# Kernel tuning notes

Measured on AMD Instinct MI355X. Metric: run time of the kernel, lower is better.

Reference implementation:

```python
import jax, jax.numpy as jnp
import numpy as np

N, E, F_IN, NUM_GRAPHS, K = 50000, 500000, 160, 128, 3


def _glorot(k, shape):
    lim = np.sqrt(6.0 / (shape[-2] + shape[-1])).astype(np.float32)
    return jax.random.uniform(k, shape, jnp.float32, -lim, lim)


def setup_inputs() -> dict:
    key = jax.random.key(0)
    ks = jax.random.split(key, 8)
    x = jax.random.normal(ks[0], (N, F_IN), jnp.float32)
    edge_index = jax.random.randint(ks[1], (2, E), 0, N)
    edge_attr = jax.random.uniform(ks[2], (E,), jnp.float32)
    batch = jnp.sort(jax.random.randint(ks[3], (N,), 0, NUM_GRAPHS))
    W1 = _glorot(ks[4], (K, F_IN, 128)); b1 = jnp.zeros((128,), jnp.float32)
    W2 = _glorot(ks[5], (K, 128, 64)); b2 = jnp.zeros((64,), jnp.float32)
    W3 = _glorot(ks[6], (K, 64, 32)); b3 = jnp.zeros((32,), jnp.float32)
    Wl = _glorot(ks[7], (32, 2)); bl = jnp.zeros((2,), jnp.float32)
    return dict(x=x, edge_index=edge_index, edge_attr=edge_attr, batch=batch,
                W1=W1, b1=b1, W2=W2, b2=b2, W3=W3, b3=b3, Wl=Wl, bl=bl)


def _cheb_norm(src, dst, edge_attr, n):
    # PyG ChebConv: sym-normalized Laplacian, lambda_max=2 =>
    # L_hat = (2/lmax)*L_sym - I = -D^{-1/2} A D^{-1/2} (diagonal = 0)
    deg = jax.ops.segment_sum(edge_attr, src, num_segments=n)
    safe = jnp.where(deg > 0, deg, 1.0)
    dinv = jnp.where(deg > 0, jax.lax.rsqrt(safe), 0.0)
    return -dinv[src] * edge_attr * dinv[dst]


def _propagate(x, src, dst, w, n):
    # out[dst] += w * x[src]  (sparse L_hat @ x)
    return jax.ops.segment_sum(w[:, None] * x[src], dst, num_segments=n)


def _cheb_conv(x, src, dst, w, W, b, n):
    # Chebyshev recurrence: T0 = x, T1 = L_hat x, Tk = 2 L_hat T(k-1) - T(k-2)
    tx0 = x
    out = tx0 @ W[0]
    tx1 = _propagate(tx0, src, dst, w, n)
    out = out + tx1 @ W[1]
    for k in range(2, W.shape[0]):
        tx2 = 2.0 * _propagate(tx1, src, dst, w, n) - tx0
        out = out + tx2 @ W[k]
        tx0, tx1 = tx1, tx2
    return out + b


def reference(x, edge_index, edge_attr, batch, W1, b1, W2, b2, W3, b3, Wl, bl):
    n = x.shape[0]
    src, dst = edge_index[0], edge_index[1]
    w = _cheb_norm(src, dst, edge_attr, n)
    h = jax.nn.relu(_cheb_conv(x, src, dst, w, W1, b1, n))
    h = jax.nn.relu(_cheb_conv(h, src, dst, w, W2, b2, n))
    h = jax.nn.relu(_cheb_conv(h, src, dst, w, W3, b3, n))
    # global_mean_pool over graph ids (dropout omitted: eval mode)
    sums = jax.ops.segment_sum(h, batch, num_segments=NUM_GRAPHS)
    cnt = jax.ops.segment_sum(jnp.ones((n,), h.dtype), batch, num_segments=NUM_GRAPHS)
    pooled = sums / jnp.maximum(cnt, 1.0)[:, None]
    return pooled @ Wl + bl
```

## Files before the change

kernel.cpp:

```cpp
#include <hip/hip_runtime.h>

#define N_NODES 50000
#define N_EDGES 500000
#define NUM_G   128
#define SCAN_NB 49
#define PN      (SCAN_NB * 1024)
#define NCX     64
#define ECH     7813
#define RNG     8192
#define NRY     7
#define HVB     (2 * NCX * NRY)
#define CONVB   7813
#define WPREPB  360
#define SCVB    (NCX * NRY)
#define GEMM_MB 782

typedef __attribute__((ext_vector_type(8))) short short8;
typedef __attribute__((ext_vector_type(4))) float f32x4;

__device__ __forceinline__ unsigned f2bf(float x) {
    unsigned u = __float_as_uint(x);
    return (u + 0x7FFFu + ((u >> 16) & 1u)) >> 16;
}
__device__ __forceinline__ float bf2f(unsigned h) {
    return __uint_as_float(h << 16);
}

__device__ __forceinline__ void wprep_one(const float* __restrict__ W, unsigned short* __restrict__ WT,
                                          int t, int FIN, int F) {
    int n = t / FIN, k = t - n * FIN;
    int sel = n / F, c = n - sel * F;
    float v;
    if (sel == 0) v = W[(size_t)k * F + c] - W[(size_t)2 * FIN * F + (size_t)k * F + c];
    else          v = W[(size_t)sel * FIN * F + (size_t)k * F + c];
    WT[t] = (unsigned short)f2bf(v);
}

__global__ __launch_bounds__(256)
void prep_kernel(const int* __restrict__ src, const int* __restrict__ dst,
                 const float* __restrict__ ea,
                 float* __restrict__ pdeg, int* __restrict__ pcnt,
                 const float* __restrict__ x, unsigned short* __restrict__ Xb,
                 const float* __restrict__ W1, const float* __restrict__ W2,
                 const float* __restrict__ W3,
                 unsigned short* __restrict__ WT1, unsigned short* __restrict__ WT2,
                 unsigned short* __restrict__ WT3) {
    __shared__ unsigned lh[RNG];
    int vb = blockIdx.x, tid = threadIdx.x;
    if (vb < HVB) {
        bool isdeg = vb < NCX * NRY;
        int v2 = isdeg ? vb : vb - NCX * NRY;
        int xk = v2 & 63, y = v2 >> 6;
        int base = y * RNG;
        for (int i = tid; i < RNG; i += 256) lh[i] = 0u;
        __syncthreads();
        int e0 = xk * ECH, e1 = min(e0 + ECH, N_EDGES);
        if (isdeg) {
            for (int e = e0 + tid; e < e1; e += 256) {
                int s = src[e];
                if ((unsigned)(s - base) < RNG) atomicAdd((float*)&lh[s - base], ea[e]);
            }
        } else {
            for (int e = e0 + tid; e < e1; e += 256) {
                int d = dst[e];
                if ((unsigned)(d - base) < RNG) atomicAdd((int*)&lh[d - base], 1);
            }
        }
        __syncthreads();
        if (isdeg) {
            for (int i = tid; i < RNG; i += 256) {
                int n = base + i;
                if (n < PN) pdeg[(size_t)xk * PN + n] = ((float*)lh)[i];
            }
        } else {
            for (int i = tid; i < RNG; i += 256) {
                int n = base + i;
                if (n < PN) pcnt[(size_t)xk * PN + n] = ((int*)lh)[i];
            }
        }
    } else if (vb < HVB + CONVB) {
        int t = (vb - HVB) * 256 + tid;
        if (t < N_NODES * 160 / 4) {
            float4 v = reinterpret_cast<const float4*>(x)[t];
            ushort4 r;
            r.x = (unsigned short)f2bf(v.x);
            r.y = (unsigned short)f2bf(v.y);
            r.z = (unsigned short)f2bf(v.z);
            r.w = (unsigned short)f2bf(v.w);
            *reinterpret_cast<ushort4*>(Xb + (size_t)t * 4) = r;
        }
    } else {
        int t = (vb - HVB - CONVB) * 256 + tid;
        if (t < 61440)      wprep_one(W1, WT1, t, 160, 128);
        else if (t < 86016) wprep_one(W2, WT2, t - 61440, 128, 64);
        else if (t < 92160) wprep_one(W3, WT3, t - 86016, 64, 32);
    }
}

__global__ __launch_bounds__(256)
void reduce_scan_kernel(const float* __restrict__ pdeg, int* __restrict__ pcnt,
                        float* __restrict__ dinv, int* __restrict__ cnt,
                        int* __restrict__ partial) {
    int b = blockIdx.x, t = threadIdx.x;
    int i0 = b * 1024 + t * 4;
    float d0 = 0.f, d1 = 0.f, d2 = 0.f, d3 = 0.f;
    int r0 = 0, r1 = 0, r2 = 0, r3 = 0;
    for (int x = 0; x < NCX; ++x) {
        float4 pv = *reinterpret_cast<const float4*>(pdeg + (size_t)x * PN + i0);
        int4   cv = *reinterpret_cast<const int4*>(pcnt + (size_t)x * PN + i0);
        *reinterpret_cast<int4*>(pcnt + (size_t)x * PN + i0) = make_int4(r0, r1, r2, r3);
        d0 += pv.x; d1 += pv.y; d2 += pv.z; d3 += pv.w;
        r0 += cv.x; r1 += cv.y; r2 += cv.z; r3 += cv.w;
    }
    float dd[4] = {d0, d1, d2, d3};
    int   rr[4] = {r0, r1, r2, r3};
    int s = 0;
    #pragma unroll
    for (int j = 0; j < 4; ++j) {
        int n = i0 + j;
        if (n < N_NODES) {
            float dv = dd[j], r = 0.f;
            if (dv > 0.f) {
                r = rsqrtf(dv);
                r = r * (1.5f - 0.5f * dv * r * r);
            }
            dinv[n] = r;
            cnt[n] = rr[j];
            s += rr[j];
        } else {
            cnt[n] = 0;
        }
    }
    __shared__ int red[256];
    red[t] = s;
    __syncthreads();
    for (int off = 128; off > 0; off >>= 1) {
        if (t < off) red[t] += red[t + off];
        __syncthreads();
    }
    if (t == 0) partial[b] = red[0];
}

__global__ __launch_bounds__(256)
void scan_final_kernel(const int* __restrict__ cnt, const int* __restrict__ partial,
                       int* __restrict__ rowptr, int n) {
    int b = blockIdx.x, t = threadIdx.x;
    __shared__ int red[256];
    __shared__ int sh_off, sh_tot;
    if (t < 64) {
        int orig = (t < SCAN_NB) ? partial[t] : 0;
        int v = orig;
        #pragma unroll
        for (int off = 1; off < 64; off <<= 1) {
            int u = __shfl_up(v, off, 64);
            if (t >= off) v += u;
        }
        if (t == b) sh_off = v - orig;
        if (t == SCAN_NB - 1) sh_tot = v;
    }
    __syncthreads();
    int4 v = reinterpret_cast<const int4*>(cnt)[b * 256 + t];
    int s = v.x + v.y + v.z + v.w;
    red[t] = s;
    __syncthreads();
    for (int off = 1; off < 256; off <<= 1) {
        int u = (t >= off) ? red[t - off] : 0;
        __syncthreads();
        red[t] += u;
        __syncthreads();
    }
    int excl = sh_off + ((t == 0) ? 0 : red[t - 1]);
    int i0 = b * 1024 + t * 4;
    if (i0 < n)     rowptr[i0]     = excl;
    if (i0 + 1 < n) rowptr[i0 + 1] = excl + v.x;
    if (i0 + 2 < n) rowptr[i0 + 2] = excl + v.x + v.y;
    if (i0 + 3 < n) rowptr[i0 + 3] = excl + v.x + v.y + v.z;
    if (b == SCAN_NB - 1 && t == 0) rowptr[n] = sh_tot;
}

__device__ void scatter_body(int vb, const int* __restrict__ src, const int* __restrict__ dst,
                             const float* __restrict__ ea,
                             const int* __restrict__ rowptr, const int* __restrict__ pcnt,
                             int2* __restrict__ csr, unsigned char* smraw) {
    int* cursor = (int*)smraw;
    int tid = threadIdx.x;
    int x = vb & 63, y = vb >> 6;
    int base = y * RNG;
    for (int i = tid; i < RNG; i += 256) {
        int n = base + i;
        cursor[i] = (n < N_NODES) ? (rowptr[n] + pcnt[(size_t)x * PN + n]) : 0;
    }
    __syncthreads();
    int e0 = x * ECH, e1 = min(e0 + ECH, N_EDGES);
    for (int e = e0 + tid; e < e1; e += 256) {
        int d = dst[e];
        if ((unsigned)(d - base) < RNG) {
            int pos = atomicAdd(&cursor[d - base], 1);
            int2 ew;
            ew.x = src[e];
            ew.y = __float_as_int(ea[e]);
            csr[pos] = ew;
        }
    }
}

template<int FIN, int F>
__device__ void gemm_body(int bx, int g, const unsigned short* __restrict__ Xb,
                          const unsigned short* __restrict__ WT, const float* __restrict__ dinv,
                          unsigned short* __restrict__ Y0, unsigned short* __restrict__ Y1,
                          unsigned short* __restrict__ Y2, int nrows, unsigned char* smraw) {
    constexpr int KT = FIN / 32;
    constexpr int NT = F / 32;
    constexpr int SA = FIN + 8;
    constexpr int F8 = FIN / 8;
    short* Bs = (short*)smraw;

    int tid = threadIdx.x;
    int lane = tid & 63, w = tid >> 6;
    int m0 = bx * 64;
    unsigned short* Ys = (g == 0) ? Y0 : (g == 1) ? Y1 : Y2;

    int colb = lane & 15;
    int q8 = (lane >> 4) << 3;
    int rq = (lane >> 4) << 2;
    int arow = m0 + w * 16 + colb;
    bool rok = arow < nrows;

    short8 afr[KT];
    #pragma unroll
    for (int kt = 0; kt < KT; ++kt) {
        short8 z = {0, 0, 0, 0, 0, 0, 0, 0};
        afr[kt] = rok ? *reinterpret_cast<const short8*>(Xb + (size_t)arow * FIN + (kt << 5) + q8) : z;
    }

    for (int nt = 0; nt < NT; ++nt) {
        int n0 = (g * NT + nt) << 5;
        __syncthreads();
        for (int span = tid; span < 32 * F8; span += 256) {
            int r = span / F8, c8 = (span - r * F8) << 3;
            int pr = (r < 16) ? (r << 1) : (((r - 16) << 1) + 1);
            *reinterpret_cast<uint4*>(&Bs[r * SA + c8]) =
                *reinterpret_cast<const uint4*>(WT + (size_t)(n0 + pr) * FIN + c8);
        }
        __syncthreads();

        f32x4 acc0 = {0.f, 0.f, 0.f, 0.f}, acc1 = acc0;
        #pragma unroll
        for (int kt = 0; kt < KT; ++kt) {
            short8 b0 = *reinterpret_cast<const short8*>(&Bs[colb * SA + (kt << 5) + q8]);
            short8 b1 = *reinterpret_cast<const short8*>(&Bs[(colb + 16) * SA + (kt << 5) + q8]);
            acc0 = __builtin_amdgcn_mfma_f32_16x16x32_bf16(afr[kt], b0, acc0, 0, 0, 0);
            acc1 = __builtin_amdgcn_mfma_f32_16x16x32_bf16(afr[kt], b1, acc1, 0, 0, 0);
        }

        int lc = (nt << 5) + (colb << 1);
        #pragma unroll
        for (int r = 0; r < 4; ++r) {
            int orow = m0 + w * 16 + rq + r;
            if (orow < nrows) {
                float sc = (g == 2) ? dinv[orow] : 1.0f;
                unsigned pack = f2bf(acc0[r] * sc) | (f2bf(acc1[r] * sc) << 16);
                *reinterpret_cast<unsigned*>(Ys + (size_t)orow * F + lc) = pack;
            }
        }
    }
}

__global__ __launch_bounds__(256)
void sg_kernel(const int* __restrict__ src, const int* __restrict__ dst,
               const float* __restrict__ ea,
               const int* __restrict__ rowptr, const int* __restrict__ pcnt,
               int2* __restrict__ csr,
               const unsigned short* __restrict__ Xb, const unsigned short* __restrict__ WT1,
               const float* __restrict__ dinv,
               unsigned short* __restrict__ Y0, unsigned short* __restrict__ Y1,
               unsigned short* __restrict__ Y2) {
    __shared__ alignas(16) unsigned char sm[32768];
    int vb = blockIdx.x;
    if (vb < SCVB) {
        scatter_body(vb, src, dst, ea, rowptr, pcnt, csr, sm);
    } else {
        int v2 = vb - SCVB;
        gemm_body<160, 128>(v2 % GEMM_MB, v2 / GEMM_MB, Xb, WT1, dinv, Y0, Y1, Y2, N_NODES, sm);
    }
}

template<int FIN, int F>
__launch_bounds__(256)
__global__ void cheb_gemm(const unsigned short* __restrict__ Xb, const unsigned short* __restrict__ WT,
                          const float* __restrict__ dinv,
                          unsigned short* __restrict__ Y0, unsigned short* __restrict__ Y1,
                          unsigned short* __restrict__ Y2, int nrows) {
    __shared__ alignas(16) unsigned char sm[32 * (FIN + 8) * 2];
    gemm_body<FIN, F>(blockIdx.x, blockIdx.y, Xb, WT, dinv, Y0, Y1, Y2, nrows, sm);
}

__device__ __forceinline__ void acc8(float* acc, uint4 p, float wv) {
    acc[0] += wv * bf2f(p.x & 0xFFFFu);
    acc[1] += wv * __uint_as_float(p.x & 0xFFFF0000u);
    acc[2] += wv * bf2f(p.y & 0xFFFFu);
    acc[3] += wv * __uint_as_float(p.y & 0xFFFF0000u);
    acc[4] += wv * bf2f(p.z & 0xFFFFu);
    acc[5] += wv * __uint_as_float(p.z & 0xFFFF0000u);
    acc[6] += wv * bf2f(p.w & 0xFFFFu);
    acc[7] += wv * __uint_as_float(p.w & 0xFFFF0000u);
}

__device__ __forceinline__ void expand8(uint4 p, float* o) {
    o[0] = bf2f(p.x & 0xFFFFu);
    o[1] = __uint_as_float(p.x & 0xFFFF0000u);
    o[2] = bf2f(p.y & 0xFFFFu);
    o[3] = __uint_as_float(p.y & 0xFFFF0000u);
    o[4] = bf2f(p.z & 0xFFFFu);
    o[5] = __uint_as_float(p.z & 0xFFFF0000u);
    o[6] = bf2f(p.w & 0xFFFFu);
    o[7] = __uint_as_float(p.w & 0xFFFF0000u);
}

template<int F, int MODE>
__launch_bounds__(256)
__global__ void gather_kernel(const unsigned short* __restrict__ X, const int2* __restrict__ csr,
                              const int* __restrict__ rowptr, const float* __restrict__ dinv,
                              const unsigned short* __restrict__ Y, const float* __restrict__ bias,
                              unsigned short* __restrict__ O, int n) {
    constexpr int FQ8 = F >> 3;
    constexpr int DPB = 256 / FQ8;
    constexpr int CAP = 2048;
    __shared__ int2 scsr[CAP];
    __shared__ int srp[DPB + 1];
    int tid = threadIdx.x;
    int db0 = blockIdx.x * DPB;
    if (tid <= DPB) srp[tid] = rowptr[min(db0 + tid, n)];
    __syncthreads();
    int ebeg = srp[0];
    int ecnt = srp[DPB] - ebeg;
    bool staged = ecnt <= CAP;
    if (staged) {
        for (int i = tid; i < ecnt; i += 256)
            scsr[i] = csr[ebeg + i];
    }
    __syncthreads();

    int d = db0 + tid / FQ8;
    if (d >= n) return;
    int f8 = (tid % FQ8) << 3;
    float acc[8] = {0.f, 0.f, 0.f, 0.f, 0.f, 0.f, 0.f, 0.f};

    if (staged) {
        int beg = srp[tid / FQ8] - ebeg, end = srp[tid / FQ8 + 1] - ebeg;
        int i = beg;
        for (; i + 7 < end; i += 8) {
            int2 e0 = scsr[i],     e1 = scsr[i + 1], e2 = scsr[i + 2], e3 = scsr[i + 3];
            int2 e4 = scsr[i + 4], e5 = scsr[i + 5], e6 = scsr[i + 6], e7 = scsr[i + 7];
            uint4 p0 = *reinterpret_cast<const uint4*>(X + (size_t)e0.x * F + f8);
            uint4 p1 = *reinterpret_cast<const uint4*>(X + (size_t)e1.x * F + f8);
            uint4 p2 = *reinterpret_cast<const uint4*>(X + (size_t)e2.x * F + f8);
            uint4 p3 = *reinterpret_cast<const uint4*>(X + (size_t)e3.x * F + f8);
            uint4 p4 = *reinterpret_cast<const uint4*>(X + (size_t)e4.x * F + f8);
            uint4 p5 = *reinterpret_cast<const uint4*>(X + (size_t)e5.x * F + f8);
            uint4 p6 = *reinterpret_cast<const uint4*>(X + (size_t)e6.x * F + f8);
            uint4 p7 = *reinterpret_cast<const uint4*>(X + (size_t)e7.x * F + f8);
            acc8(acc, p0, __int_as_float(e0.y));
            acc8(acc, p1, __int_as_float(e1.y));
            acc8(acc, p2, __int_as_float(e2.y));
            acc8(acc, p3, __int_as_float(e3.y));
            acc8(acc, p4, __int_as_float(e4.y));
            acc8(acc, p5, __int_as_float(e5.y));
            acc8(acc, p6, __int_as_float(e6.y));
            acc8(acc, p7, __int_as_float(e7.y));
        }
        for (; i + 3 < end; i += 4) {
            int2 e0 = scsr[i], e1 = scsr[i + 1], e2 = scsr[i + 2], e3 = scsr[i + 3];
            uint4 p0 = *reinterpret_cast<const uint4*>(X + (size_t)e0.x * F + f8);
            uint4 p1 = *reinterpret_cast<const uint4*>(X + (size_t)e1.x * F + f8);
            uint4 p2 = *reinterpret_cast<const uint4*>(X + (size_t)e2.x * F + f8);
            uint4 p3 = *reinterpret_cast<const uint4*>(X + (size_t)e3.x * F + f8);
            acc8(acc, p0, __int_as_float(e0.y));
            acc8(acc, p1, __int_as_float(e1.y));
            acc8(acc, p2, __int_as_float(e2.y));
            acc8(acc, p3, __int_as_float(e3.y));
        }
        for (; i < end; ++i) {
            int2 e = scsr[i];
            uint4 p = *reinterpret_cast<const uint4*>(X + (size_t)e.x * F + f8);
            acc8(acc, p, __int_as_float(e.y));
        }
    } else {
        int beg = srp[tid / FQ8], end = srp[tid / FQ8 + 1];
        for (int i = beg; i < end; ++i) {
            int2 e = csr[i];
            uint4 p = *reinterpret_cast<const uint4*>(X + (size_t)e.x * F + f8);
            acc8(acc, p, __int_as_float(e.y));
        }
    }

    float y[8];
    expand8(*reinterpret_cast<const uint4*>(Y + (size_t)d * F + f8), y);
    float dv = dinv[d];
    float v[8];
    if (MODE == 0) {
        float dv2 = 2.f * dv;
        #pragma unroll
        for (int j = 0; j < 8; ++j) v[j] = dv * (y[j] - dv2 * acc[j]);
    } else {
        float4 ba = *reinterpret_cast<const float4*>(bias + f8);
        float4 bb = *reinterpret_cast<const float4*>(bias + f8 + 4);
        v[0] = fmaxf(y[0] - dv * acc[0] + ba.x, 0.f);
        v[1] = fmaxf(y[1] - dv * acc[1] + ba.y, 0.f);
        v[2] = fmaxf(y[2] - dv * acc[2] + ba.z, 0.f);
        v[3] = fmaxf(y[3] - dv * acc[3] + ba.w, 0.f);
        v[4] = fmaxf(y[4] - dv * acc[4] + bb.x, 0.f);
        v[5] = fmaxf(y[5] - dv * acc[5] + bb.y, 0.f);
        v[6] = fmaxf(y[6] - dv * acc[6] + bb.z, 0.f);
        v[7] = fmaxf(y[7] - dv * acc[7] + bb.w, 0.f);
    }
    uint4 o;
    o.x = f2bf(v[0]) | (f2bf(v[1]) << 16);
    o.y = f2bf(v[2]) | (f2bf(v[3]) << 16);
    o.z = f2bf(v[4]) | (f2bf(v[5]) << 16);
    o.w = f2bf(v[6]) | (f2bf(v[7]) << 16);
    *reinterpret_cast<uint4*>(O + (size_t)d * F + f8) = o;
}

__device__ __forceinline__ int lower_bound_dev(const int* __restrict__ a, int n, int v) {
    int lo = 0, hi = n;
    while (lo < hi) {
        int mid = (lo + hi) >> 1;
        if (a[mid] < v) lo = mid + 1; else hi = mid;
    }
    return lo;
}

__global__ void pool_kernel(const unsigned short* __restrict__ H, const int* __restrict__ batch,
                            const float* __restrict__ Wl, const float* __restrict__ bl,
                            float* __restrict__ out, int n) {
    int g = blockIdx.x;
    int start = lower_bound_dev(batch, n, g);
    int end   = lower_bound_dev(batch, n, g + 1);
    int tid = threadIdx.x;
    int f = tid & 31;
    int sub = tid >> 5;
    float acc = 0.0f;
    for (int i = start + sub; i < end; i += 8)
        acc += bf2f((unsigned)H[(size_t)i * 32 + f]);
    __shared__ float red[256];
    red[tid] = acc;
    __syncthreads();
    if (tid < 128) red[tid] += red[tid + 128];
    __syncthreads();
    if (tid < 64) red[tid] += red[tid + 64];
    __syncthreads();
    if (tid < 32) red[tid] += red[tid + 32];
    __syncthreads();
    if (tid < 2) {
        int cnt = end - start;
        float inv = 1.0f / (float)(cnt > 0 ? cnt : 1);
        float o = bl[tid];
        for (int f2 = 0; f2 < 32; ++f2)
            o += red[f2] * inv * Wl[f2 * 2 + tid];
        out[g * 2 + tid] = o;
    }
}

extern "C" void kernel_launch(void* const* d_in, const int* in_sizes, int n_in,
                              void* d_out, int out_size, void* d_ws, size_t ws_size,
                              hipStream_t stream) {
    const float* x     = (const float*)d_in[0];
    const int*   ei    = (const int*)d_in[1];
    const float* ea    = (const float*)d_in[2];
    const int*   batch = (const int*)d_in[3];
    const float* W1 = (const float*)d_in[4];
    const float* b1 = (const float*)d_in[5];
    const float* W2 = (const float*)d_in[6];
    const float* b2 = (const float*)d_in[7];
    const float* W3 = (const float*)d_in[8];
    const float* b3 = (const float*)d_in[9];
    const float* Wl = (const float*)d_in[10];
    const float* bl = (const float*)d_in[11];
    float* out = (float*)d_out;
    char* ws = (char*)d_ws;

    const int* src = ei;
    const int* dst = ei + N_EDGES;

    size_t off = 0;
    auto alloc = [&](size_t bytes) { char* p = ws + off; off += (bytes + 255) & ~(size_t)255; return p; };
    float* pdeg    = (float*)alloc((size_t)NCX * PN * 4);
    int*   pcnt    = (int*)  alloc((size_t)NCX * PN * 4);
    float* dinv    = (float*)alloc(N_NODES * 4);
    int*   cnt     = (int*)  alloc((size_t)PN * 4);
    int*   partial = (int*)  alloc(SCAN_NB * 4);
    int*   rowptr  = (int*)  alloc((N_NODES + 1) * 4);
    int2*  csr     = (int2*) alloc((size_t)N_EDGES * 8);
    unsigned short* Xb  = (unsigned short*)alloc((size_t)N_NODES * 160 * 2);
    unsigned short* Y0  = (unsigned short*)alloc((size_t)N_NODES * 128 * 2);
    unsigned short* Y1  = (unsigned short*)alloc((size_t)N_NODES * 128 * 2);
    unsigned short* Y2  = (unsigned short*)alloc((size_t)N_NODES * 128 * 2);
    unsigned short* U   = (unsigned short*)alloc((size_t)N_NODES * 128 * 2);
    unsigned short* WT1 = (unsigned short*)alloc((size_t)384 * 160 * 2);
    unsigned short* WT2 = (unsigned short*)alloc((size_t)192 * 128 * 2);
    unsigned short* WT3 = (unsigned short*)alloc((size_t)96 * 64 * 2);

    const int BT = 256;

    prep_kernel<<<HVB + CONVB + WPREPB, BT, 0, stream>>>(src, dst, ea, pdeg, pcnt,
                                                         x, Xb, W1, W2, W3, WT1, WT2, WT3);
    reduce_scan_kernel<<<SCAN_NB, BT, 0, stream>>>(pdeg, pcnt, dinv, cnt, partial);
    scan_final_kernel<<<SCAN_NB, BT, 0, stream>>>(cnt, partial, rowptr, N_NODES);
    sg_kernel<<<SCVB + 3 * GEMM_MB, BT, 0, stream>>>(src, dst, ea, rowptr, pcnt, csr,
                                                     Xb, WT1, dinv, Y0, Y1, Y2);

    dim3 ggrid(GEMM_MB, 3);
    auto gb = [&](int F) { int DPB = 256 / (F / 8); return (N_NODES + DPB - 1) / DPB; };

    gather_kernel<128, 0><<<gb(128), BT, 0, stream>>>(Y2, csr, rowptr, dinv, Y1, nullptr, U, N_NODES);
    gather_kernel<128, 1><<<gb(128), BT, 0, stream>>>(U, csr, rowptr, dinv, Y0, b1, Xb, N_NODES);

    cheb_gemm<128, 64><<<ggrid, BT, 0, stream>>>(Xb, WT2, dinv, Y0, Y1, Y2, N_NODES);
    gather_kernel<64, 0><<<gb(64), BT, 0, stream>>>(Y2, csr, rowptr, dinv, Y1, nullptr, U, N_NODES);
    gather_kernel<64, 1><<<gb(64), BT, 0, stream>>>(U, csr, rowptr, dinv, Y0, b2, Xb, N_NODES);

    cheb_gemm<64, 32><<<ggrid, BT, 0, stream>>>(Xb, WT3, dinv, Y0, Y1, Y2, N_NODES);
    gather_kernel<32, 0><<<gb(32), BT, 0, stream>>>(Y2, csr, rowptr, dinv, Y1, nullptr, U, N_NODES);
    gather_kernel<32, 1><<<gb(32), BT, 0, stream>>>(U, csr, rowptr, dinv, Y0, b3, Xb, N_NODES);

    pool_kernel<<<NUM_G, BT, 0, stream>>>(Xb, batch, Wl, bl, out, N_NODES);
}
```

Measured before the change: 312.0 us.

## Replace LDS-privatized edge histograms with direct global atomics for degree and CSR build

```diff
diff --git a/kernel.cpp b/kernel.cpp
--- a/kernel.cpp
+++ b/kernel.cpp
@@ -5,15 +5,11 @@
 #define NUM_G   128
 #define SCAN_NB 49
 #define PN      (SCAN_NB * 1024)
-#define NCX     64
-#define ECH     7813
-#define RNG     8192
-#define NRY     7
-#define HVB     (2 * NCX * NRY)
+#define EB      489
 #define CONVB   7813
 #define WPREPB  360
-#define SCVB    (NCX * NRY)
 #define GEMM_MB 782
+#define ZB      98
 
 typedef __attribute__((ext_vector_type(8))) short short8;
 typedef __attribute__((ext_vector_type(4))) float f32x4;
@@ -24,6 +20,13 @@
 }
 __device__ __forceinline__ float bf2f(unsigned h) {
     return __uint_as_float(h << 16);
+}
+
+__global__ __launch_bounds__(256)
+void zero_kernel(float* __restrict__ p) {
+    int i = (blockIdx.x * 256 + threadIdx.x) * 4;
+    if (i < 2 * PN)
+        *reinterpret_cast<float4*>(p + i) = make_float4(0.f, 0.f, 0.f, 0.f);
 }
 
 __device__ __forceinline__ void wprep_one(const float* __restrict__ W, unsigned short* __restrict__ WT,
@@ -39,47 +42,30 @@
 __global__ __launch_bounds__(256)
 void prep_kernel(const int* __restrict__ src, const int* __restrict__ dst,
                  const float* __restrict__ ea,
-                 float* __restrict__ pdeg, int* __restrict__ pcnt,
+                 float* __restrict__ deg, int* __restrict__ cnt,
                  const float* __restrict__ x, unsigned short* __restrict__ Xb,
                  const float* __restrict__ W1, const float* __restrict__ W2,
                  const float* __restrict__ W3,
                  unsigned short* __restrict__ WT1, unsigned short* __restrict__ WT2,
                  unsigned short* __restrict__ WT3) {
-    __shared__ unsigned lh[RNG];
     int vb = blockIdx.x, tid = threadIdx.x;
-    if (vb < HVB) {
-        bool isdeg = vb < NCX * NRY;
-        int v2 = isdeg ? vb : vb - NCX * NRY;
-        int xk = v2 & 63, y = v2 >> 6;
-        int base = y * RNG;
-        for (int i = tid; i < RNG; i += 256) lh[i] = 0u;
-        __syncthreads();
-        int e0 = xk * ECH, e1 = min(e0 + ECH, N_EDGES);
-        if (isdeg) {
-            for (int e = e0 + tid; e < e1; e += 256) {
-                int s = src[e];
-                if ((unsigned)(s - base) < RNG) atomicAdd((float*)&lh[s - base], ea[e]);
-            }
-        } else {
-            for (int e = e0 + tid; e < e1; e += 256) {
-                int d = dst[e];
-                if ((unsigned)(d - base) < RNG) atomicAdd((int*)&lh[d - base], 1);
-            }
-        }
-        __syncthreads();
-        if (isdeg) {
-            for (int i = tid; i < RNG; i += 256) {
-                int n = base + i;
-                if (n < PN) pdeg[(size_t)xk * PN + n] = ((float*)lh)[i];
-            }
-        } else {
-            for (int i = tid; i < RNG; i += 256) {
-                int n = base + i;
-                if (n < PN) pcnt[(size_t)xk * PN + n] = ((int*)lh)[i];
-            }
-        }
-    } else if (vb < HVB + CONVB) {
-        int t = (vb - HVB) * 256 + tid;
+    if (vb < EB) {
+        int e0 = vb * 1024 + tid * 4;
+        if (e0 < N_EDGES) {
+            int4   s4 = *reinterpret_cast<const int4*>(src + e0);
+            int4   d4 = *reinterpret_cast<const int4*>(dst + e0);
+            float4 w4 = *reinterpret_cast<const float4*>(ea + e0);
+            atomicAdd(deg + s4.x, w4.x);
+            atomicAdd(deg + s4.y, w4.y);
+            atomicAdd(deg + s4.z, w4.z);
+            atomicAdd(deg + s4.w, w4.w);
+            atomicAdd(cnt + d4.x, 1);
+            atomicAdd(cnt + d4.y, 1);
+            atomicAdd(cnt + d4.z, 1);
+            atomicAdd(cnt + d4.w, 1);
+        }
+    } else if (vb < EB + CONVB) {
+        int t = (vb - EB) * 256 + tid;
         if (t < N_NODES * 160 / 4) {
             float4 v = reinterpret_cast<const float4*>(x)[t];
             ushort4 r;
@@ -90,7 +76,7 @@
             *reinterpret_cast<ushort4*>(Xb + (size_t)t * 4) = r;
         }
     } else {
-        int t = (vb - HVB - CONVB) * 256 + tid;
+        int t = (vb - EB - CONVB) * 256 + tid;
         if (t < 61440)      wprep_one(W1, WT1, t, 160, 128);
         else if (t < 86016) wprep_one(W2, WT2, t - 61440, 128, 64);
         else if (t < 92160) wprep_one(W3, WT3, t - 86016, 64, 32);
@@ -98,39 +84,26 @@
 }
 
 __global__ __launch_bounds__(256)
-void reduce_scan_kernel(const float* __restrict__ pdeg, int* __restrict__ pcnt,
-                        float* __restrict__ dinv, int* __restrict__ cnt,
-                        int* __restrict__ partial) {
+void finalize_kernel(const float* __restrict__ deg, const int* __restrict__ cnt,
+                     float* __restrict__ dinv, int* __restrict__ partial) {
     int b = blockIdx.x, t = threadIdx.x;
     int i0 = b * 1024 + t * 4;
-    float d0 = 0.f, d1 = 0.f, d2 = 0.f, d3 = 0.f;
-    int r0 = 0, r1 = 0, r2 = 0, r3 = 0;
-    for (int x = 0; x < NCX; ++x) {
-        float4 pv = *reinterpret_cast<const float4*>(pdeg + (size_t)x * PN + i0);
-        int4   cv = *reinterpret_cast<const int4*>(pcnt + (size_t)x * PN + i0);
-        *reinterpret_cast<int4*>(pcnt + (size_t)x * PN + i0) = make_int4(r0, r1, r2, r3);
-        d0 += pv.x; d1 += pv.y; d2 += pv.z; d3 += pv.w;
-        r0 += cv.x; r1 += cv.y; r2 += cv.z; r3 += cv.w;
-    }
-    float dd[4] = {d0, d1, d2, d3};
-    int   rr[4] = {r0, r1, r2, r3};
-    int s = 0;
+    float4 dv4 = *reinterpret_cast<const float4*>(deg + i0);
+    int4   cv  = *reinterpret_cast<const int4*>(cnt + i0);
+    float dd[4] = {dv4.x, dv4.y, dv4.z, dv4.w};
     #pragma unroll
     for (int j = 0; j < 4; ++j) {
         int n = i0 + j;
         if (n < N_NODES) {
-            float dv = dd[j], r = 0.f;
-            if (dv > 0.f) {
-                r = rsqrtf(dv);
-                r = r * (1.5f - 0.5f * dv * r * r);
+            float d = dd[j], r = 0.f;
+            if (d > 0.f) {
+                r = rsqrtf(d);
+                r = r * (1.5f - 0.5f * d * r * r);
             }
             dinv[n] = r;
-            cnt[n] = rr[j];
-            s += rr[j];
-        } else {
-            cnt[n] = 0;
-        }
-    }
+        }
+    }
+    int s = cv.x + cv.y + cv.z + cv.w;
     __shared__ int red[256];
     red[t] = s;
     __syncthreads();
@@ -143,7 +116,7 @@
 
 __global__ __launch_bounds__(256)
 void scan_final_kernel(const int* __restrict__ cnt, const int* __restrict__ partial,
-                       int* __restrict__ rowptr, int n) {
+                       int* __restrict__ rowptr, int* __restrict__ cursor, int n) {
     int b = blockIdx.x, t = threadIdx.x;
     __shared__ int red[256];
     __shared__ int sh_off, sh_tot;
@@ -171,37 +144,12 @@
     }
     int excl = sh_off + ((t == 0) ? 0 : red[t - 1]);
     int i0 = b * 1024 + t * 4;
-    if (i0 < n)     rowptr[i0]     = excl;
-    if (i0 + 1 < n) rowptr[i0 + 1] = excl + v.x;
-    if (i0 + 2 < n) rowptr[i0 + 2] = excl + v.x + v.y;
-    if (i0 + 3 < n) rowptr[i0 + 3] = excl + v.x + v.y + v.z;
+    int e0 = excl, e1 = excl + v.x, e2 = excl + v.x + v.y, e3 = excl + v.x + v.y + v.z;
+    if (i0 < n)     { rowptr[i0]     = e0; cursor[i0]     = e0; }
+    if (i0 + 1 < n) { rowptr[i0 + 1] = e1; cursor[i0 + 1] = e1; }
+    if (i0 + 2 < n) { rowptr[i0 + 2] = e2; cursor[i0 + 2] = e2; }
+    if (i0 + 3 < n) { rowptr[i0 + 3] = e3; cursor[i0 + 3] = e3; }
     if (b == SCAN_NB - 1 && t == 0) rowptr[n] = sh_tot;
-}
-
-__device__ void scatter_body(int vb, const int* __restrict__ src, const int* __restrict__ dst,
-                             const float* __restrict__ ea,
-                             const int* __restrict__ rowptr, const int* __restrict__ pcnt,
-                             int2* __restrict__ csr, unsigned char* smraw) {
-    int* cursor = (int*)smraw;
-    int tid = threadIdx.x;
-    int x = vb & 63, y = vb >> 6;
-    int base = y * RNG;
-    for (int i = tid; i < RNG; i += 256) {
-        int n = base + i;
-        cursor[i] = (n < N_NODES) ? (rowptr[n] + pcnt[(size_t)x * PN + n]) : 0;
-    }
-    __syncthreads();
-    int e0 = x * ECH, e1 = min(e0 + ECH, N_EDGES);
-    for (int e = e0 + tid; e < e1; e += 256) {
-        int d = dst[e];
-        if ((unsigned)(d - base) < RNG) {
-            int pos = atomicAdd(&cursor[d - base], 1);
-            int2 ew;
-            ew.x = src[e];
-            ew.y = __float_as_int(ea[e]);
-            csr[pos] = ew;
-        }
-    }
 }
 
 template<int FIN, int F>
@@ -269,18 +217,29 @@
 __global__ __launch_bounds__(256)
 void sg_kernel(const int* __restrict__ src, const int* __restrict__ dst,
                const float* __restrict__ ea,
-               const int* __restrict__ rowptr, const int* __restrict__ pcnt,
-               int2* __restrict__ csr,
+               int* __restrict__ cursor, int2* __restrict__ csr,
                const unsigned short* __restrict__ Xb, const unsigned short* __restrict__ WT1,
                const float* __restrict__ dinv,
                unsigned short* __restrict__ Y0, unsigned short* __restrict__ Y1,
                unsigned short* __restrict__ Y2) {
-    __shared__ alignas(16) unsigned char sm[32768];
+    __shared__ alignas(16) unsigned char sm[32 * (160 + 8) * 2];
     int vb = blockIdx.x;
-    if (vb < SCVB) {
-        scatter_body(vb, src, dst, ea, rowptr, pcnt, csr, sm);
+    if (vb < EB) {
+        int tid = threadIdx.x;
+        int e0 = vb * 1024 + tid * 4;
+        if (e0 < N_EDGES) {
+            int4   s4 = *reinterpret_cast<const int4*>(src + e0);
+            int4   d4 = *reinterpret_cast<const int4*>(dst + e0);
+            float4 w4 = *reinterpret_cast<const float4*>(ea + e0);
+            int2 ew;
+            int p;
+            p = atomicAdd(cursor + d4.x, 1); ew.x = s4.x; ew.y = __float_as_int(w4.x); csr[p] = ew;
+            p = atomicAdd(cursor + d4.y, 1); ew.x = s4.y; ew.y = __float_as_int(w4.y); csr[p] = ew;
+            p = atomicAdd(cursor + d4.z, 1); ew.x = s4.z; ew.y = __float_as_int(w4.z); csr[p] = ew;
+            p = atomicAdd(cursor + d4.w, 1); ew.x = s4.w; ew.y = __float_as_int(w4.w); csr[p] = ew;
+        }
     } else {
-        int v2 = vb - SCVB;
+        int v2 = vb - EB;
         gemm_body<160, 128>(v2 % GEMM_MB, v2 / GEMM_MB, Xb, WT1, dinv, Y0, Y1, Y2, N_NODES, sm);
     }
 }
@@ -485,12 +444,12 @@
 
     size_t off = 0;
     auto alloc = [&](size_t bytes) { char* p = ws + off; off += (bytes + 255) & ~(size_t)255; return p; };
-    float* pdeg    = (float*)alloc((size_t)NCX * PN * 4);
-    int*   pcnt    = (int*)  alloc((size_t)NCX * PN * 4);
+    float* deg     = (float*)alloc((size_t)PN * 4);
+    int*   cnt     = (int*)  alloc((size_t)PN * 4);
     float* dinv    = (float*)alloc(N_NODES * 4);
-    int*   cnt     = (int*)  alloc((size_t)PN * 4);
     int*   partial = (int*)  alloc(SCAN_NB * 4);
     int*   rowptr  = (int*)  alloc((N_NODES + 1) * 4);
+    int*   cursor  = (int*)  alloc((size_t)N_NODES * 4);
     int2*  csr     = (int2*) alloc((size_t)N_EDGES * 8);
     unsigned short* Xb  = (unsigned short*)alloc((size_t)N_NODES * 160 * 2);
     unsigned short* Y0  = (unsigned short*)alloc((size_t)N_NODES * 128 * 2);
@@ -503,12 +462,13 @@
 
     const int BT = 256;
 
-    prep_kernel<<<HVB + CONVB + WPREPB, BT, 0, stream>>>(src, dst, ea, pdeg, pcnt,
-                                                         x, Xb, W1, W2, W3, WT1, WT2, WT3);
-    reduce_scan_kernel<<<SCAN_NB, BT, 0, stream>>>(pdeg, pcnt, dinv, cnt, partial);
-    scan_final_kernel<<<SCAN_NB, BT, 0, stream>>>(cnt, partial, rowptr, N_NODES);
-    sg_kernel<<<SCVB + 3 * GEMM_MB, BT, 0, stream>>>(src, dst, ea, rowptr, pcnt, csr,
-                                                     Xb, WT1, dinv, Y0, Y1, Y2);
+    zero_kernel<<<ZB, BT, 0, stream>>>(deg);
+    prep_kernel<<<EB + CONVB + WPREPB, BT, 0, stream>>>(src, dst, ea, deg, cnt,
+                                                        x, Xb, W1, W2, W3, WT1, WT2, WT3);
+    finalize_kernel<<<SCAN_NB, BT, 0, stream>>>(deg, cnt, dinv, partial);
+    scan_final_kernel<<<SCAN_NB, BT, 0, stream>>>(cnt, partial, rowptr, cursor, N_NODES);
+    sg_kernel<<<EB + 3 * GEMM_MB, BT, 0, stream>>>(src, dst, ea, cursor, csr,
+                                                   Xb, WT1, dinv, Y0, Y1, Y2);
 
     dim3 ggrid(GEMM_MB, 3);
     auto gb = [&](int F) { int DPB = 256 / (F / 8); return (N_NODES + DPB - 1) / DPB; };
```

After: 331.0 us. 1.06x slower.
